# Kernel tuning notes

Measured on AMD Instinct MI355X. Metric: run time of the kernel, lower is better.

## Reference

```python
import jax, jax.numpy as jnp
import numpy as np

T, B, H, L = 128, 64, 1024, 4


def setup_inputs() -> dict:
    key = jax.random.key(0)
    k1, k2, k3 = jax.random.split(key, 3)
    inputs = jax.random.normal(k1, (T, B, H), dtype=jnp.float32)
    W = jax.random.normal(k2, (L, H, 4 * H), dtype=jnp.float32) * 0.02
    U = jax.random.normal(k3, (L, H, 4 * H), dtype=jnp.float32) * 0.02
    b = jnp.zeros((L, 4 * H), dtype=jnp.float32)
    return {"inputs": inputs, "W": W, "U": U, "b": b}


def _lstm_cell(x, h_prev, c_prev, Wj, Uj, bj):
    # Standard keras LSTMCell math: z = x@W + h@U + b, gates order i,f,g,o
    z = x @ Wj + h_prev @ Uj + bj  # [B, 4H]
    i, f, g, o = jnp.split(z, 4, axis=-1)
    c = jax.nn.sigmoid(f) * c_prev + jax.nn.sigmoid(i) * jnp.tanh(g)
    h = jax.nn.sigmoid(o) * jnp.tanh(c)
    return h, c


def reference(inputs, W, U, b):
    n_layers = W.shape[0]
    batch = inputs.shape[1]
    hidden = W.shape[1]
    # state_c in the original holds hidden states (a), state_h holds cell states (bb)
    a0 = jnp.zeros((n_layers, batch, hidden), dtype=inputs.dtype)
    b0 = jnp.zeros((n_layers, batch, hidden), dtype=inputs.dtype)

    def step(carry, x):
        a, bb = carry
        cur = x
        for j in range(n_layers):  # static, small layer loop
            # original passes (c, h) to keras cell -> h_tm1 = a[j], c_tm1 = bb[j]
            h, c = _lstm_cell(cur, a[j], bb[j], W[j], U[j], b[j])
            a = a.at[j].set(h)
            bb = bb.at[j].set(c)
            cur = c  # original feeds the new CELL state to the next layer
        return (a, bb), None

    (a, bb), _ = jax.lax.scan(step, (a0, b0), inputs)
    # original returns state_h.read(num_layers-1) == final cell state of last layer
    return bb[n_layers - 1]
```

## Files before the change

### kernel.cpp

```cpp
#include <hip/hip_runtime.h>

#define TT 128
#define BB 64
#define HH 1024
#define LL 4
#define NWG 256

typedef _Float16 f16;
typedef __attribute__((ext_vector_type(4))) _Float16 f16x4;
typedef __attribute__((ext_vector_type(8))) _Float16 f16x8;
typedef __attribute__((ext_vector_type(4))) float f32x4;
typedef unsigned long long u64;

__device__ __align__(16) f16 g_in16[TT][65536];
__device__ __align__(16) f16 g_c16[LL][4][65536];
__device__ __align__(16) f16 g_h16[LL][4][65536];
__device__ __align__(16) float g_c32[LL][BB][HH];
__device__ unsigned g_ep[LL][64];

__global__ void k_init() {
  unsigned tid = blockIdx.x * blockDim.x + threadIdx.x;
  unsigned n = gridDim.x * blockDim.x;
  float* c32 = &g_c32[0][0][0];
  for (unsigned i = tid; i < LL * BB * HH; i += n) c32[i] = 0.f;
  for (unsigned i = tid; i < LL * 32768; i += n) {
    int jj = i >> 15, q = i & 32767;
    ((unsigned*)&g_h16[jj][0][0])[q] = 0u;
  }
  unsigned* pe = &g_ep[0][0];
  for (unsigned i = tid; i < LL * 64; i += n) pe[i] = 0u;
}

__global__ void k_pack_in(const float* __restrict__ inp) {
  int tid = blockIdx.x * blockDim.x + threadIdx.x;
  int t = tid >> 14, q = tid & 16383;
  int row = q >> 8, hu = (q & 255) << 2;
  const float4 x = *(const float4*)(inp + ((size_t)t << 16) + (row << 10) + hu);
  int rg = row >> 4, ktp = hu >> 5;
  int ln = (((hu >> 2) & 3) << 4) | (row & 15);
  int e0 = ((hu >> 4) & 1) << 2;
  f16x4 v = {(f16)x.x, (f16)x.y, (f16)x.z, (f16)x.w};
  *(f16x4*)&g_in16[t][(((rg * 32 + ktp) * 64 + ln) << 3) + e0] = v;
}

__device__ __forceinline__ float sigf(float x) { return 1.f / (1.f + __expf(-x)); }
__device__ __forceinline__ float tanh_(float x) {
  float q = __expf(-2.f * fabsf(x));
  return copysignf((1.f - q) / (1.f + q), x);
}
__device__ __forceinline__ f16x4 lo8(f16x8 v) { return __builtin_shufflevector(v, v, 0, 1, 2, 3); }
__device__ __forceinline__ f16x4 hi8(f16x8 v) { return __builtin_shufflevector(v, v, 4, 5, 6, 7); }
__device__ __forceinline__ void waitep(const unsigned* ep, unsigned target) {
  for (;;) {
    unsigned e = __hip_atomic_load(ep, __ATOMIC_RELAXED, __HIP_MEMORY_SCOPE_AGENT);
    if (__all((int)(e >= target))) break;
    __builtin_amdgcn_s_sleep(1);
  }
}
__device__ __forceinline__ f16x8 ldA(const f16* p, bool coh) {
  if (coh) {
    const u64* q = (const u64*)p;
    union { u64 v[2]; f16x8 h; } u;
    u.v[0] = __hip_atomic_load(q,     __ATOMIC_RELAXED, __HIP_MEMORY_SCOPE_AGENT);
    u.v[1] = __hip_atomic_load(q + 1, __ATOMIC_RELAXED, __HIP_MEMORY_SCOPE_AGENT);
    return u.h;
  }
  return *(const f16x8*)p;
}

#define MFMA16(A_, B_, C_) __builtin_amdgcn_mfma_f32_16x16x16f16(A_, B_, C_, 0, 0, 0)
#define SWZ(r) ((((r) & 4) << 2) ^ (((r) & 3) << 3))

__global__ __launch_bounds__(512, 2) void k_main(const float* __restrict__ W,
                                                 const float* __restrict__ U,
                                                 const float* __restrict__ bias,
                                                 float* __restrict__ out) {
  const int j = blockIdx.x >> 6, s = blockIdx.x & 63;
  const int tid = threadIdx.x, lane = tid & 63, wv = tid >> 6;
  const int mat = wv >> 2, kq = wv & 3;
  __shared__ float zl[16384];

  const float* src = (mat ? U : W) + (size_t)j * (HH * 4 * HH);
  const int colb = s * 16 + (lane & 15);
  const int kb0 = kq * 256 + ((lane >> 4) << 2);
  f16x8 Wr[32];
#pragma unroll
  for (int kk = 0; kk < 16; ++kk)
#pragma unroll
    for (int cfp = 0; cfp < 2; ++cfp) {
      f16x8 v;
#pragma unroll
      for (int hf = 0; hf < 2; ++hf)
#pragma unroll
        for (int e = 0; e < 4; ++e)
          v[hf * 4 + e] = (f16)src[(size_t)(kb0 + kk * 16 + e) * 4096 + (cfp * 2 + hf) * 1024 + colb];
      Wr[kk * 2 + cfp] = v;
    }

  const bool act = tid < 256;
  const int row = (tid & 255) >> 2;
  const int hl0q = (tid & 3) * 4;
  const int hu0 = s * 16 + hl0q;
  f32x4 brg[4];
#pragma unroll
  for (int g = 0; g < 4; ++g) brg[g] = *(const f32x4*)&bias[j * 4096 + g * 1024 + hu0];
  const int grp = (((row >> 4) * 32 + (hu0 >> 5)) * 64 +
                   ((((hu0 >> 2) & 3) << 4) | (row & 15)));
  const int e0 = ((hu0 >> 4) & 1) << 2;
  const int g64 = grp * 2 + (e0 >> 2);
  u64* const hP = (u64*)&g_h16[j][0][0];
  u64* const cP = (u64*)&g_c16[j][0][0];
  float* const c32p = &g_c32[j][row][hu0];
  const int ktp0 = kq * 8;
  const bool coh = mat || (j > 0);
  const unsigned* epX = (j > 0) ? &g_ep[j - 1][kq * 16 + (lane & 15)] : nullptr;
  const unsigned* epH = &g_ep[j][kq * 16 + (lane & 15)];
  const unsigned* epA = (j < 3) ? &g_ep[j + 1][lane] : nullptr;

  for (int t = 0; t < TT; ++t) {
    if (mat == 0) {
      if (j > 0) waitep(epX, (unsigned)(t + 1));
    } else {
      if (t > 0) waitep(epH, (unsigned)t);
      if (j < 3 && t >= 2) waitep(epA, (unsigned)(t - 2));
    }
    asm volatile("" ::: "memory");

    const f16* Ab = mat ? &g_h16[j][t & 3][0]
                        : (j ? &g_c16[j - 1][(t + 1) & 3][0] : &g_in16[t][0]);
    f16x8 a[2][4];
#pragma unroll
    for (int rf = 0; rf < 4; ++rf)
      a[0][rf] = ldA(Ab + (rf * 32 + ktp0) * 512 + lane * 8, coh);

    f32x4 acc[4][4];
#pragma unroll
    for (int rf = 0; rf < 4; ++rf)
#pragma unroll
      for (int cf = 0; cf < 4; ++cf) acc[rf][cf] = (f32x4){0.f, 0.f, 0.f, 0.f};

#pragma unroll
    for (int kc = 0; kc < 8; ++kc) {
      if (kc < 7) {
#pragma unroll
        for (int rf = 0; rf < 4; ++rf)
          a[(kc + 1) & 1][rf] = ldA(Ab + (rf * 32 + ktp0 + kc + 1) * 512 + lane * 8, coh);
      }
#pragma unroll
      for (int hf = 0; hf < 2; ++hf) {
        f16x4 a4[4];
#pragma unroll
        for (int rf = 0; rf < 4; ++rf)
          a4[rf] = hf ? hi8(a[kc & 1][rf]) : lo8(a[kc & 1][rf]);
#pragma unroll
        for (int cf = 0; cf < 4; ++cf) {
          const f16x8 wreg = Wr[(kc * 2 + hf) * 2 + (cf >> 1)];
          const f16x4 b4 = (cf & 1) ? hi8(wreg) : lo8(wreg);
#pragma unroll
          for (int rf = 0; rf < 4; ++rf) acc[rf][cf] = MFMA16(a4[rf], b4, acc[rf][cf]);
        }
      }
    }

    float gsum[4][4];
#pragma unroll
    for (int P = 0; P < 2; ++P) {
      __syncthreads();
#pragma unroll
      for (int rf = 0; rf < 4; ++rf)
#pragma unroll
        for (int ch = 0; ch < 2; ++ch) {
          const int cf = P * 2 + ch;
#pragma unroll
          for (int ri = 0; ri < 4; ++ri) {
            const int rr = rf * 16 + ((lane >> 4) << 2) + ri;
            const int c2 = ch * 16 + (lane & 15);
            zl[wv * 2048 + rr * 32 + (c2 ^ SWZ(rr))] = acc[rf][cf][ri];
          }
        }
      __syncthreads();
      if (act) {
#pragma unroll
        for (int ch = 0; ch < 2; ++ch) {
          const int g = P * 2 + ch;
          const int swcol = (ch * 16 + hl0q) ^ SWZ(row);
          f32x4 ss = (f32x4){0.f, 0.f, 0.f, 0.f};
#pragma unroll
          for (int w = 0; w < 8; ++w) ss += *(const f32x4*)&zl[w * 2048 + row * 32 + swcol];
#pragma unroll
          for (int el = 0; el < 4; ++el) gsum[el][g] = ss[el];
        }
      }
    }

    if (act) {
      const f32x4 cp = *(const f32x4*)c32p;
      f32x4 cn, hn;
#pragma unroll
      for (int el = 0; el < 4; ++el) {
        const float zi = gsum[el][0] + brg[0][el];
        const float zf = gsum[el][1] + brg[1][el];
        const float zg = gsum[el][2] + brg[2][el];
        const float zo = gsum[el][3] + brg[3][el];
        cn[el] = sigf(zf) * cp[el] + sigf(zi) * tanh_(zg);
        hn[el] = sigf(zo) * tanh_(cn[el]);
      }
      *(f32x4*)c32p = cn;
      union { f16 h[4]; u64 u; } ph, pc;
#pragma unroll
      for (int el = 0; el < 4; ++el) { ph.h[el] = (f16)hn[el]; pc.h[el] = (f16)cn[el]; }
      const int slot = (t + 1) & 3;
      __hip_atomic_store(hP + (size_t)slot * 16384 + g64, ph.u,
                         __ATOMIC_RELAXED, __HIP_MEMORY_SCOPE_AGENT);
      if (j < 3)
        __hip_atomic_store(cP + (size_t)slot * 16384 + g64, pc.u,
                           __ATOMIC_RELAXED, __HIP_MEMORY_SCOPE_AGENT);
      if (j == 3 && t == TT - 1) *(f32x4*)&out[(row << 10) + hu0] = cn;
    }

    asm volatile("s_waitcnt vmcnt(0)" ::: "memory");
    __syncthreads();
    if (tid == 0)
      __hip_atomic_store(&g_ep[j][s], (unsigned)(t + 1),
                         __ATOMIC_RELAXED, __HIP_MEMORY_SCOPE_AGENT);
  }
}

extern "C" void kernel_launch(void* const* d_in, const int* in_sizes, int n_in,
                              void* d_out, int out_size, void* d_ws, size_t ws_size,
                              hipStream_t stream) {
  const float* inp  = (const float*)d_in[0];
  const float* W    = (const float*)d_in[1];
  const float* U    = (const float*)d_in[2];
  const float* bias = (const float*)d_in[3];
  float* out = (float*)d_out;
  k_init<<<256, 256, 0, stream>>>();
  k_pack_in<<<4096, 512, 0, stream>>>(inp);
  k_main<<<NWG, 512, 0, stream>>>(W, U, bias, out);
}
```

Measured before the change: 2.121 ms.

## Mirror recurrent activations into per-XCD copies before MFMA reads

Each timestep, the workgroups on the same XCD cooperatively copy the freshly produced h and c activation tiles from the global coherent buffers into a per-XCD mirror. A per-XCD counter barrier follows, and the MFMA A-operand loads then use plain non-atomic loads from the mirror, which is meant to hit the local L2 instead of doing agent-scope coherent loads. The epoch wait is also consolidated into one wave that polls all 64 producers, followed by a block barrier. This adds an extra copy pass, a second grid-level barrier per step, and a startup election barrier. It also relies on plain loads of the mirror not returning stale cached lines across timesteps, which is a correctness risk.

```diff
diff --git a/kernel.cpp b/kernel.cpp
--- a/kernel.cpp
+++ b/kernel.cpp
@@ -17,6 +17,10 @@
 __device__ __align__(16) f16 g_h16[LL][4][65536];
 __device__ __align__(16) float g_c32[LL][BB][HH];
 __device__ unsigned g_ep[LL][64];
+__device__ __align__(16) f16 g_mir[8][LL][4][2][65536];
+__device__ unsigned g_elect[LL][8];
+__device__ unsigned g_arrive;
+__device__ unsigned g_mep[8][LL];
 
 __global__ void k_init() {
   unsigned tid = blockIdx.x * blockDim.x + threadIdx.x;
@@ -29,6 +33,11 @@
   }
   unsigned* pe = &g_ep[0][0];
   for (unsigned i = tid; i < LL * 64; i += n) pe[i] = 0u;
+  unsigned* pl = &g_elect[0][0];
+  for (unsigned i = tid; i < LL * 8; i += n) pl[i] = 0u;
+  unsigned* pm = &g_mep[0][0];
+  for (unsigned i = tid; i < 8 * LL; i += n) pm[i] = 0u;
+  if (tid == 0) g_arrive = 0u;
 }
 
 __global__ void k_pack_in(const float* __restrict__ inp) {
@@ -50,22 +59,12 @@
 }
 __device__ __forceinline__ f16x4 lo8(f16x8 v) { return __builtin_shufflevector(v, v, 0, 1, 2, 3); }
 __device__ __forceinline__ f16x4 hi8(f16x8 v) { return __builtin_shufflevector(v, v, 4, 5, 6, 7); }
-__device__ __forceinline__ void waitep(const unsigned* ep, unsigned target) {
-  for (;;) {
-    unsigned e = __hip_atomic_load(ep, __ATOMIC_RELAXED, __HIP_MEMORY_SCOPE_AGENT);
-    if (__all((int)(e >= target))) break;
-    __builtin_amdgcn_s_sleep(1);
-  }
-}
-__device__ __forceinline__ f16x8 ldA(const f16* p, bool coh) {
-  if (coh) {
-    const u64* q = (const u64*)p;
-    union { u64 v[2]; f16x8 h; } u;
-    u.v[0] = __hip_atomic_load(q,     __ATOMIC_RELAXED, __HIP_MEMORY_SCOPE_AGENT);
-    u.v[1] = __hip_atomic_load(q + 1, __ATOMIC_RELAXED, __HIP_MEMORY_SCOPE_AGENT);
-    return u.h;
-  }
-  return *(const f16x8*)p;
+__device__ __forceinline__ f16x8 ldA(const f16* p) {
+  const u64* q = (const u64*)p;
+  union { u64 v[2]; f16x8 h; } u;
+  u.v[0] = __hip_atomic_load(q,     __ATOMIC_RELAXED, __HIP_MEMORY_SCOPE_AGENT);
+  u.v[1] = __hip_atomic_load(q + 1, __ATOMIC_RELAXED, __HIP_MEMORY_SCOPE_AGENT);
+  return u.h;
 }
 
 #define MFMA16(A_, B_, C_) __builtin_amdgcn_mfma_f32_16x16x16f16(A_, B_, C_, 0, 0, 0)
@@ -79,6 +78,11 @@
   const int tid = threadIdx.x, lane = tid & 63, wv = tid >> 6;
   const int mat = wv >> 2, kq = wv & 3;
   __shared__ float zl[16384];
+  __shared__ unsigned shinfo[2];
+
+  unsigned xcd;
+  asm("s_getreg_b32 %0, hwreg(HW_REG_XCC_ID)" : "=s"(xcd));
+  xcd &= 7u;
 
   const float* src = (mat ? U : W) + (size_t)j * (HH * 4 * HH);
   const int colb = s * 16 + (lane & 15);
@@ -96,6 +100,18 @@
           v[hf * 4 + e] = (f16)src[(size_t)(kb0 + kk * 16 + e) * 4096 + (cfp * 2 + hf) * 1024 + colb];
       Wr[kk * 2 + cfp] = v;
     }
+
+  if (tid == 0) {
+    unsigned tk = __hip_atomic_fetch_add(&g_elect[j][xcd], 1u,
+                                         __ATOMIC_RELAXED, __HIP_MEMORY_SCOPE_AGENT);
+    __hip_atomic_fetch_add(&g_arrive, 1u, __ATOMIC_RELAXED, __HIP_MEMORY_SCOPE_AGENT);
+    while (__hip_atomic_load(&g_arrive, __ATOMIC_RELAXED, __HIP_MEMORY_SCOPE_AGENT) < NWG)
+      __builtin_amdgcn_s_sleep(2);
+    shinfo[0] = tk;
+    shinfo[1] = __hip_atomic_load(&g_elect[j][xcd], __ATOMIC_RELAXED, __HIP_MEMORY_SCOPE_AGENT);
+  }
+  __syncthreads();
+  const unsigned ticket = shinfo[0], nfill = shinfo[1];
 
   const bool act = tid < 256;
   const int row = (tid & 255) >> 2;
@@ -112,26 +128,57 @@
   u64* const cP = (u64*)&g_c16[j][0][0];
   float* const c32p = &g_c32[j][row][hu0];
   const int ktp0 = kq * 8;
-  const bool coh = mat || (j > 0);
-  const unsigned* epX = (j > 0) ? &g_ep[j - 1][kq * 16 + (lane & 15)] : nullptr;
-  const unsigned* epH = &g_ep[j][kq * 16 + (lane & 15)];
-  const unsigned* epA = (j < 3) ? &g_ep[j + 1][lane] : nullptr;
 
   for (int t = 0; t < TT; ++t) {
-    if (mat == 0) {
-      if (j > 0) waitep(epX, (unsigned)(t + 1));
-    } else {
-      if (t > 0) waitep(epH, (unsigned)t);
-      if (j < 3 && t >= 2) waitep(epA, (unsigned)(t - 2));
-    }
-    asm volatile("" ::: "memory");
-
-    const f16* Ab = mat ? &g_h16[j][t & 3][0]
-                        : (j ? &g_c16[j - 1][(t + 1) & 3][0] : &g_in16[t][0]);
+    const int rs = t & 3;
+
+    if (wv == 0) {
+      const bool nx = (j > 0), nh = (t > 0), na = (j < 3 && t >= 2);
+      if (nx | nh | na) {
+        for (;;) {
+          bool ok = true;
+          if (nx) ok &= (__hip_atomic_load(&g_ep[j - 1][lane], __ATOMIC_RELAXED,
+                                           __HIP_MEMORY_SCOPE_AGENT) >= (unsigned)(t + 1));
+          if (nh) ok &= (__hip_atomic_load(&g_ep[j][lane], __ATOMIC_RELAXED,
+                                           __HIP_MEMORY_SCOPE_AGENT) >= (unsigned)t);
+          if (na) ok &= (__hip_atomic_load(&g_ep[j + 1][lane], __ATOMIC_RELAXED,
+                                           __HIP_MEMORY_SCOPE_AGENT) >= (unsigned)(t - 2));
+          if (__all((int)ok)) break;
+          __builtin_amdgcn_s_sleep(1);
+        }
+      }
+    }
+    __syncthreads();
+
+    {
+      f16* const mbase = &g_mir[xcd][j][rs][0][0];
+      for (unsigned k = ticket; k < 16u; k += nfill) {
+        if (j == 0 && k < 8u) continue;
+        const int mk = (int)(k >> 3), sub = (int)(k & 7);
+        const f16* sp = (mk ? &g_h16[j][rs][0] : &g_c16[j - 1][(t + 1) & 3][0])
+                        + sub * 8192 + tid * 16;
+        f16* dp = mbase + mk * 65536 + sub * 8192 + tid * 16;
+        f16x8 v0 = ldA(sp), v1 = ldA(sp + 8);
+        *(f16x8*)dp = v0;
+        *(f16x8*)(dp + 8) = v1;
+      }
+    }
+    asm volatile("s_waitcnt vmcnt(0)" ::: "memory");
+    __syncthreads();
+    if (tid == 0) {
+      __hip_atomic_fetch_add(&g_mep[xcd][j], 1u, __ATOMIC_RELAXED, __HIP_MEMORY_SCOPE_AGENT);
+      while (__hip_atomic_load(&g_mep[xcd][j], __ATOMIC_RELAXED,
+                               __HIP_MEMORY_SCOPE_AGENT) < nfill * (unsigned)(t + 1))
+        __builtin_amdgcn_s_sleep(1);
+    }
+    __syncthreads();
+
+    const f16* Ab = mat ? &g_mir[xcd][j][rs][1][0]
+                        : (j ? &g_mir[xcd][j][rs][0][0] : &g_in16[t][0]);
     f16x8 a[2][4];
 #pragma unroll
     for (int rf = 0; rf < 4; ++rf)
-      a[0][rf] = ldA(Ab + (rf * 32 + ktp0) * 512 + lane * 8, coh);
+      a[0][rf] = *(const f16x8*)(Ab + (rf * 32 + ktp0) * 512 + lane * 8);
 
     f32x4 acc[4][4];
 #pragma unroll
@@ -144,7 +191,7 @@
       if (kc < 7) {
 #pragma unroll
         for (int rf = 0; rf < 4; ++rf)
-          a[(kc + 1) & 1][rf] = ldA(Ab + (rf * 32 + ktp0 + kc + 1) * 512 + lane * 8, coh);
+          a[(kc + 1) & 1][rf] = *(const f16x8*)(Ab + (rf * 32 + ktp0 + kc + 1) * 512 + lane * 8);
       }
 #pragma unroll
       for (int hf = 0; hf < 2; ++hf) {
```

Result: slower. 2.949 ms (+39.1%).
